# Kernel tuning notes

Hardware: AMD Instinct MI355X
Metric: run time of the kernel (lower is better)

The kernel has to match this reference:

```python
import jax, jax.numpy as jnp
import numpy as np

B, NP1, D = 64, 1025, 256  # N+1 tokens, feature dim d (label dim makes d+1)
N_LAYER, N_HEAD = 4, 4
VAR = 0.02


def _pad_pq(allparam):
    """Build padded (d+1)x(d+1) P_full/Q_full for all layers/heads at once.
    P_full gets a 1 at [d, d]; Q_full is zero-padded."""
    L, H, _, d, _ = allparam.shape
    Pf = (jnp.zeros((L, H, d + 1, d + 1), allparam.dtype)
          .at[:, :, :d, :d].set(allparam[:, :, 0])
          .at[:, :, d, d].set(1.0))
    Qf = (jnp.zeros((L, H, d + 1, d + 1), allparam.dtype)
          .at[:, :, :d, :d].set(allparam[:, :, 1]))
    return Pf, Qf


def setup_inputs() -> dict:
    key = jax.random.key(0)
    k1, k2 = jax.random.split(key)
    Z = jax.random.normal(k1, (B, NP1, D + 1), dtype=jnp.float32)
    allparam = jax.random.normal(k2, (N_LAYER, N_HEAD, 2, D, D), dtype=jnp.float32) * VAR
    return {"Z": Z, "allparam": allparam}


def reference(Z, allparam):
    Bb, Np1, dp1 = Z.shape
    N = Np1 - 1
    Pf, Qf = _pad_pq(allparam)  # (L, H, d+1, d+1)
    # mask A = diag(1,...,1,0): equivalent to zeroing the last key token
    mask = jnp.ones((Np1,), Z.dtype).at[N].set(0.0)
    for l in range(allparam.shape[0]):
        # attn[b,h,n,m] = Z[b,n,:] @ Q_full[h] @ Z[b,m,:]
        attn = jnp.einsum('bni,hij,bmj->bhnm', Z, Qf[l], Z)
        attn = jax.nn.relu(attn)
        # key[b,h,m,i] = P_full[h] @ Z[b,m,:], last token masked out (A matrix)
        key_t = jnp.einsum('hij,bmj->bhmi', Pf[l], Z) * mask[None, None, :, None]
        # sum over heads fused into the einsum reduction; scale by 1/N
        res = jnp.einsum('bhnm,bhmi->bni', attn, key_t) / N
        Z = Z + res  # residual connection
    return Z
```

## Files before the change

### kernel.cpp

```cpp
#include <hip/hip_runtime.h>
#include <cstdint>
#include <cstddef>

#define B_    64
#define NP1   1025
#define N_    1024
#define D_    256
#define DP1   257
#define L_    4
#define H_    4
#define MT    1024
#define NCHE  32
#define IPAD  272
#define TR_   1024

typedef __bf16 bf16;
typedef bf16 bf16x4 __attribute__((ext_vector_type(4)));
typedef bf16 bf16x8 __attribute__((ext_vector_type(8)));
typedef float f32x4 __attribute__((ext_vector_type(4)));

__device__ __forceinline__ f32x4 mfma16(bf16x8 a, bf16x8 b, f32x4 c) {
    return __builtin_amdgcn_mfma_f32_16x16x32_bf16(a, b, c, 0, 0, 0);
}

__device__ __forceinline__ void async16(const void* g, void* l) {
    __builtin_amdgcn_global_load_lds(
        (const __attribute__((address_space(1))) void*)g,
        (__attribute__((address_space(3))) void*)l, 16, 0, 0);
}

__global__ void k_prep_pq(const float* __restrict__ ap,
                          bf16* __restrict__ Pb, bf16* __restrict__ Qt) {
    int idx = blockIdx.x * 256 + threadIdx.x;
    int j  = idx & 255;
    int i  = (idx >> 8) & 255;
    int lh = idx >> 16;
    const float* base = ap + (size_t)lh * 2 * D_ * D_;
    float p = base[i * D_ + j];
    float q = base[D_ * D_ + i * D_ + j];
    Pb[((size_t)lh * D_ + i) * D_ + j] = (bf16)p;
    Qt[((size_t)lh * D_ + j) * D_ + i] = (bf16)q;
}

__global__ __launch_bounds__(256) void k_zbt(const float* __restrict__ Z,
                                             bf16* __restrict__ Zb,
                                             bf16* __restrict__ ZbT) {
    __shared__ float t[64][65];
    int m0 = blockIdx.x * 64, j0 = blockIdx.y * 64, b = blockIdx.z;
    int c = threadIdx.x & 63, r0 = threadIdx.x >> 6;
#pragma unroll
    for (int s = 0; s < 16; s++) {
        int r = s * 4 + r0;
        int j = j0 + c;
        float v = (j < DP1) ? Z[((size_t)b * NP1 + m0 + r) * DP1 + j] : 0.f;
        t[r][c] = v;
        if (j < D_) Zb[((size_t)b * N_ + m0 + r) * D_ + j] = (bf16)v;
    }
    __syncthreads();
#pragma unroll
    for (int s = 0; s < 16; s++) {
        int rr = s * 4 + r0;
        int j = j0 + rr;
        if (j < DP1)
            ZbT[((size_t)b * DP1 + j) * MT + m0 + c] = (bf16)t[c][rr];
    }
}

__global__ __launch_bounds__(512, 1) void k_attn(const bf16* __restrict__ Zb,
                                                 const bf16* __restrict__ ZbT,
                                                 const bf16* __restrict__ Qt,
                                                 const bf16* __restrict__ Pb,
                                                 float* __restrict__ Z,
                                                 bf16* __restrict__ T,
                                                 bf16* __restrict__ Tlab,
                                                 int layer) {
    __shared__ bf16 zbS[2][32][256];
    __shared__ bf16 ztS[2][IPAD][32];
    __shared__ bf16 sl[8][32][40];

    const int tid  = threadIdx.x;
    const int id   = blockIdx.x;
    const int wave = tid >> 6, lane = tid & 63;
    const int quad = lane >> 4, l16 = lane & 15;

    const int xcd = id & 7, u = id >> 3;
    const int b   = xcd + 8 * (u & 7);
    const int bx  = u >> 3;
    const int n0w = bx * 256 + wave * 32;

    const bf16* Zbb  = Zb  + (size_t)b * N_ * D_;
    const bf16* ZbTb = ZbT + (size_t)b * DP1 * MT;

    const int zrow  = wave * 2 + (lane >> 5);
    const int zscol = ((lane & 31) ^ (zrow & 7)) * 8;
    const int krow  = wave * 16 + (lane >> 2);
    const int kscol = ((lane & 3) ^ ((lane >> 3) & 3)) * 8;
    const int xs    = l16 & 7;
    const int kf    = (l16 >> 1) & 3;

    auto stage = [&](int mc_, int p_) {
        int m0 = mc_ * 32;
        const bf16* zsrc = Zbb + (size_t)(m0 + zrow) * D_ + zscol;
#pragma unroll
        for (int t = 0; t < 2; t++)
            async16(zsrc + (size_t)t * 16 * D_, &zbS[p_][t * 16 + wave * 2][0]);
        const bf16* ksrc = ZbTb + (size_t)krow * MT + m0 + kscol;
#pragma unroll
        for (int t = 0; t < 2; t++)
            async16(ksrc + (size_t)t * 128 * MT, &ztS[p_][t * 128 + wave * 16][0]);
        if (wave == 0)
            async16(ksrc + (size_t)256 * MT, &ztS[p_][256][0]);
    };

    int p = 0;

    for (int h = 0; h < H_; h++) {
        const bf16* Qth = Qt + (size_t)(layer * H_ + h) * D_ * D_;

        if (h == 0) stage(0, 0);

        f32x4 acc[2][17];
#pragma unroll
        for (int ns = 0; ns < 2; ns++)
#pragma unroll
            for (int it = 0; it < 17; it++) acc[ns][it] = (f32x4){0.f, 0.f, 0.f, 0.f};

        bf16x8 zqa[2][8];
#pragma unroll 2
        for (int jc = 0; jc < 8; jc++) {
            f32x4 c00 = (f32x4){0.f,0.f,0.f,0.f}, c01 = c00, c10 = c00, c11 = c00;
#pragma unroll
            for (int kc = 0; kc < 8; kc++) {
                const bf16* qb = Qth + (size_t)(jc * 32 + l16) * D_ + kc * 32 + quad * 8;
                const bf16* az = Zbb + (size_t)(n0w + l16) * D_ + kc * 32 + quad * 8;
                bf16x8 q0 = *(const bf16x8*)(qb);
                bf16x8 q1 = *(const bf16x8*)(qb + 16 * D_);
                bf16x8 a0 = *(const bf16x8*)(az);
                bf16x8 a1 = *(const bf16x8*)(az + 16 * D_);
                c00 = mfma16(q0, a0, c00);
                c01 = mfma16(q0, a1, c01);
                c10 = mfma16(q1, a0, c10);
                c11 = mfma16(q1, a1, c11);
            }
            f32x4 cv[2][2] = {{c00, c01}, {c10, c11}};
#pragma unroll
            for (int jt = 0; jt < 2; jt++)
#pragma unroll
                for (int ns = 0; ns < 2; ns++) {
                    bf16x4 pk;
#pragma unroll
                    for (int r = 0; r < 4; r++) pk[r] = (bf16)cv[jt][ns][r];
                    *(bf16x4*)(&sl[wave][ns * 16 + l16][jt * 16 + quad * 4]) = pk;
                }
#pragma unroll
            for (int ns = 0; ns < 2; ns++)
                zqa[ns][jc] = *(const bf16x8*)(&sl[wave][ns * 16 + l16][quad * 8]);
        }

        if (h == 0) {
            asm volatile("s_waitcnt vmcnt(0)" ::: "memory");
            __builtin_amdgcn_s_barrier();
            __builtin_amdgcn_sched_barrier(0);
        }

        for (int cc = 0; cc < NCHE; cc++) {
            const bool haveNext = (cc + 1 < NCHE);
            if (haveNext) {
                int mcn = (h & 1) ? (NCHE - 2 - cc) : (cc + 1);
                stage(mcn, p ^ 1);
                if (wave == 0) asm volatile("s_waitcnt vmcnt(5)" ::: "memory");
                else           asm volatile("s_waitcnt vmcnt(4)" ::: "memory");
            } else {
                asm volatile("s_waitcnt vmcnt(0)" ::: "memory");
            }
            __builtin_amdgcn_s_barrier();
            __builtin_amdgcn_sched_barrier(0);

#pragma unroll
            for (int mt = 0; mt < 2; mt++) {
                f32x4 st0 = (f32x4){0.f,0.f,0.f,0.f}, st1 = st0;
                const bf16* zr = &zbS[p][mt * 16 + l16][0];
                __builtin_amdgcn_s_setprio(1);
#pragma unroll
                for (int kc = 0; kc < 8; kc++) {
                    bf16x8 az = *(const bf16x8*)(zr + (((kc * 4 + quad) ^ xs) * 8));
                    st0 = mfma16(az, zqa[0][kc], st0);
                    st1 = mfma16(az, zqa[1][kc], st1);
                }
                __builtin_amdgcn_s_setprio(0);
                bf16x4 p0, p1;
#pragma unroll
                for (int r = 0; r < 4; r++) {
                    p0[r] = (bf16)(st0[r] > 0.f ? st0[r] : 0.f);
                    p1[r] = (bf16)(st1[r] > 0.f ? st1[r] : 0.f);
                }
                *(bf16x4*)(&sl[wave][l16][mt * 16 + quad * 4])      = p0;
                *(bf16x4*)(&sl[wave][16 + l16][mt * 16 + quad * 4]) = p1;
            }
            bf16x8 sfrag[2];
#pragma unroll
            for (int ns = 0; ns < 2; ns++)
                sfrag[ns] = *(const bf16x8*)(&sl[wave][ns * 16 + l16][quad * 8]);

            __builtin_amdgcn_s_setprio(1);
#pragma unroll
            for (int it = 0; it < 17; it++) {
                const bf16* kr = &ztS[p][it * 16 + l16][0];
                bf16x8 bk = *(const bf16x8*)(kr + ((quad ^ kf) * 8));
                acc[0][it] = mfma16(sfrag[0], bk, acc[0][it]);
                acc[1][it] = mfma16(sfrag[1], bk, acc[1][it]);
            }
            __builtin_amdgcn_s_setprio(0);

            __builtin_amdgcn_sched_barrier(0);
            __builtin_amdgcn_s_barrier();
            if (haveNext) p ^= 1;
        }

        bf16* Th  = T    + (size_t)(b * H_ + h) * TR_ * D_;
        bf16* Tlh = Tlab + (size_t)(b * H_ + h) * TR_;
#pragma unroll
        for (int ns = 0; ns < 2; ns++)
#pragma unroll
            for (int it = 0; it < 17; it++)
#pragma unroll
                for (int r = 0; r < 4; r++) {
                    int n = n0w + ns * 16 + quad * 4 + r;
                    float v = acc[ns][it][r];
                    if (it < 16)
                        Th[(size_t)n * D_ + it * 16 + l16] = (bf16)v;
                    else if (l16 == 0)
                        Tlh[n] = (bf16)v;
                }
    }

    if (bx == 0) {
        __syncthreads();
        float* lz1 = (float*)&zbS[0][0][0];
        float* lzq = lz1 + 256;
        float* lsS = lzq + 1024;
        float* lT  = lsS + 4096;
        if (tid < 256) lz1[tid] = Z[((size_t)b * NP1 + N_) * DP1 + tid];
        __syncthreads();
        {
            int j = tid & 255, hh = tid >> 8;
            for (int h2 = hh; h2 < H_; h2 += 2) {
                const bf16* qr = Qt + ((size_t)(layer * H_ + h2) * D_ + j) * D_;
                float a = 0.f;
                for (int i8 = 0; i8 < 32; i8++) {
                    bf16x8 q = *(const bf16x8*)(qr + i8 * 8);
#pragma unroll
                    for (int k = 0; k < 8; k++) a += lz1[i8 * 8 + k] * (float)q[k];
                }
                lzq[h2 * 256 + j] = a;
            }
        }
        __syncthreads();
        for (int m = tid; m < N_; m += 512) {
            const bf16* zr = Zbb + (size_t)m * D_;
            float a0 = 0.f, a1 = 0.f, a2 = 0.f, a3 = 0.f;
            for (int j8 = 0; j8 < 32; j8++) {
                bf16x8 z8 = *(const bf16x8*)(zr + j8 * 8);
#pragma unroll
                for (int k = 0; k < 8; k++) {
                    float zv = (float)z8[k];
                    int j = j8 * 8 + k;
                    a0 += lzq[j] * zv;
                    a1 += lzq[256 + j] * zv;
                    a2 += lzq[512 + j] * zv;
                    a3 += lzq[768 + j] * zv;
                }
            }
            lsS[m]        = a0 > 0.f ? a0 : 0.f;
            lsS[1024 + m] = a1 > 0.f ? a1 : 0.f;
            lsS[2048 + m] = a2 > 0.f ? a2 : 0.f;
            lsS[3072 + m] = a3 > 0.f ? a3 : 0.f;
        }
        __syncthreads();
        if (tid < DP1) {
            const bf16* tr2 = ZbTb + (size_t)tid * MT;
            float t0 = 0.f, t1 = 0.f, t2 = 0.f, t3 = 0.f;
            for (int m8 = 0; m8 < 128; m8++) {
                bf16x8 t8 = *(const bf16x8*)(tr2 + m8 * 8);
#pragma unroll
                for (int k = 0; k < 8; k++) {
                    float zv = (float)t8[k];
                    int m = m8 * 8 + k;
                    t0 += lsS[m] * zv;
                    t1 += lsS[1024 + m] * zv;
                    t2 += lsS[2048 + m] * zv;
                    t3 += lsS[3072 + m] * zv;
                }
            }
            lT[tid] = t0; lT[257 + tid] = t1; lT[514 + tid] = t2; lT[771 + tid] = t3;
        }
        __syncthreads();
        const float inv = 1.0f / (float)N_;
        if (tid < 256) {
            float out = 0.f;
            for (int h2 = 0; h2 < H_; h2++) {
                const bf16* pr = Pb + ((size_t)(layer * H_ + h2) * D_ + tid) * D_;
                for (int j8 = 0; j8 < 32; j8++) {
                    bf16x8 p8 = *(const bf16x8*)(pr + j8 * 8);
#pragma unroll
                    for (int k = 0; k < 8; k++)
                        out += lT[h2 * 257 + j8 * 8 + k] * (float)p8[k];
                }
            }
            Z[((size_t)b * NP1 + N_) * DP1 + tid] += out * inv;
        } else if (tid == 256) {
            float lab = lT[256] + lT[513] + lT[770] + lT[1027];
            Z[((size_t)b * NP1 + N_) * DP1 + D_] += lab * inv;
        }
    }
}

__global__ __launch_bounds__(256, 4) void k_post(const bf16* __restrict__ T,
                                                 const bf16* __restrict__ Tlab,
                                                 const bf16* __restrict__ Pb,
                                                 float* __restrict__ Z,
                                                 bf16* __restrict__ Zb,
                                                 bf16* __restrict__ ZbT,
                                                 int layer) {
    const int tid  = threadIdx.x;
    const int id   = blockIdx.x;
    const int wave = tid >> 6, lane = tid & 63;
    const int quad = lane >> 4, l16 = lane & 15;
    const int xcd = id & 7, u = id >> 3;
    const int b   = xcd + 8 * (u & 3) + 32 * ((u >> 5) & 1);
    const int bx  = (u >> 2) & 7;
    const int ih  = u >> 6;
    const int n0w = bx * 128 + wave * 32;
    const int i0  = ih * 128;

    f32x4 acc[2][8];
#pragma unroll
    for (int ns = 0; ns < 2; ns++)
#pragma unroll
        for (int it = 0; it < 8; it++) acc[ns][it] = (f32x4){0.f, 0.f, 0.f, 0.f};

    for (int h = 0; h < H_; h++) {
        const bf16* Th = T  + (size_t)(b * H_ + h) * TR_ * D_;
        const bf16* Ph = Pb + (size_t)(layer * H_ + h) * D_ * D_;
#pragma unroll 2
        for (int kc = 0; kc < 8; kc++) {
            bf16x8 af[2];
#pragma unroll
            for (int ns = 0; ns < 2; ns++) {
                int row = n0w + ns * 16 + l16;
                af[ns] = *(const bf16x8*)(Th + (size_t)row * D_ + kc * 32 + quad * 8);
            }
#pragma unroll
            for (int it = 0; it < 8; it++) {
                bf16x8 bp = *(const bf16x8*)(Ph + (size_t)(i0 + it * 16 + l16) * D_ + kc * 32 + quad * 8);
                acc[0][it] = mfma16(af[0], bp, acc[0][it]);
                acc[1][it] = mfma16(af[1], bp, acc[1][it]);
            }
        }
    }

    const float inv = 1.0f / (float)N_;
    const bool wnext = (layer < L_ - 1);
#pragma unroll
    for (int ns = 0; ns < 2; ns++)
#pragma unroll
        for (int it = 0; it < 8; it++) {
            const int i = i0 + it * 16 + l16;
            const int nbase = n0w + ns * 16 + quad * 4;
            bf16x4 zpk;
#pragma unroll
            for (int r = 0; r < 4; r++) {
                int n = nbase + r;
                size_t zi = ((size_t)b * NP1 + n) * DP1 + i;
                float v = Z[zi] + acc[ns][it][r] * inv;
                Z[zi] = v;
                zpk[r] = (bf16)v;
                if (wnext) Zb[((size_t)b * N_ + n) * D_ + i] = (bf16)v;
            }
            if (wnext)
                *(bf16x4*)(&ZbT[((size_t)b * DP1 + i) * MT + nbase]) = zpk;
        }
    if (ih == 0 && tid < 128) {
        int n = bx * 128 + tid;
        float s = 0.f;
#pragma unroll
        for (int h = 0; h < H_; h++)
            s += (float)Tlab[(size_t)(b * H_ + h) * TR_ + n];
        size_t zi = ((size_t)b * NP1 + n) * DP1 + D_;
        float v = Z[zi] + s * inv;
        Z[zi] = v;
        if (wnext) ZbT[((size_t)b * DP1 + D_) * MT + n] = (bf16)v;
    }
}

extern "C" void kernel_launch(void* const* d_in, const int* in_sizes, int n_in,
                              void* d_out, int out_size, void* d_ws, size_t ws_size,
                              hipStream_t stream) {
    const float* Zin = (const float*)d_in[0];
    const float* ap  = (const float*)d_in[1];
    float* Z = (float*)d_out;

    char* ws = (char*)d_ws;
    const size_t sz_Zb  = (size_t)B_ * N_ * D_ * sizeof(bf16);
    const size_t sz_ZbT = (size_t)B_ * DP1 * MT * sizeof(bf16);
    const size_t sz_T   = (size_t)B_ * H_ * TR_ * D_ * sizeof(bf16);
    const size_t sz_Tl  = (size_t)B_ * H_ * TR_ * sizeof(bf16);
    const size_t sz_P   = (size_t)L_ * H_ * D_ * D_ * sizeof(bf16);
    bf16* Zb  = (bf16*)ws;
    bf16* ZbT = (bf16*)(ws + sz_Zb);
    bf16* Tb  = (bf16*)(ws + sz_Zb + sz_ZbT);
    bf16* Tl  = (bf16*)(ws + sz_Zb + sz_ZbT + sz_T);
    bf16* Pb  = (bf16*)(ws + sz_Zb + sz_ZbT + sz_T + sz_Tl);
    bf16* Qt  = (bf16*)(ws + sz_Zb + sz_ZbT + sz_T + sz_Tl + sz_P);

    hipMemcpyAsync(Z, Zin, (size_t)B_ * NP1 * DP1 * sizeof(float),
                   hipMemcpyDeviceToDevice, stream);

    k_prep_pq<<<dim3((L_ * H_ * D_ * D_) / 256), 256, 0, stream>>>(ap, Pb, Qt);
    k_zbt<<<dim3(N_ / 64, 5, B_), 256, 0, stream>>>(Z, Zb, ZbT);

    for (int l = 0; l < L_; l++) {
        k_attn<<<dim3(256), 512, 0, stream>>>(Zb, ZbT, Qt, Pb, Z, Tb, Tl, l);
        k_post<<<dim3(1024), 256, 0, stream>>>(Tb, Tl, Pb, Z, Zb, ZbT, l);
    }
}
```

Measured before the change: 3.326 ms.

## Fuse P-projection residual update into attention kernel and regenerate bf16 copies with k_zbt

This removes the separate k_post kernel. Each attention block now runs the P-projection over its own 256 token rows right after writing T, and adds the result into Z in place, including the label column. The bf16 copies Zb and ZbT for the next layer are no longer written by the epilogue. Instead the existing k_zbt transpose kernel is launched between layers. The aim is to save a launch and the global round trip of the separate post pass. In exchange, the projection now runs on only 256 blocks instead of 1024, and a 128-float accumulator per thread may raise register pressure.

```diff
diff --git a/kernel.cpp b/kernel.cpp
--- a/kernel.cpp
+++ b/kernel.cpp
@@ -232,6 +232,57 @@
                     else if (l16 == 0)
                         Tlh[n] = (bf16)v;
                 }
+    }
+
+    __syncthreads();
+    {
+        f32x4 acc2[2][16];
+#pragma unroll
+        for (int ns = 0; ns < 2; ns++)
+#pragma unroll
+            for (int it = 0; it < 16; it++) acc2[ns][it] = (f32x4){0.f, 0.f, 0.f, 0.f};
+
+        for (int h = 0; h < H_; h++) {
+            const bf16* Th = T  + (size_t)(b * H_ + h) * TR_ * D_;
+            const bf16* Ph = Pb + (size_t)(layer * H_ + h) * D_ * D_;
+#pragma unroll 2
+            for (int kc = 0; kc < 8; kc++) {
+                bf16x8 af[2];
+#pragma unroll
+                for (int ns = 0; ns < 2; ns++) {
+                    int row = n0w + ns * 16 + l16;
+                    af[ns] = *(const bf16x8*)(Th + (size_t)row * D_ + kc * 32 + quad * 8);
+                }
+#pragma unroll
+                for (int it = 0; it < 16; it++) {
+                    bf16x8 bp = *(const bf16x8*)(Ph + (size_t)(it * 16 + l16) * D_ + kc * 32 + quad * 8);
+                    acc2[0][it] = mfma16(af[0], bp, acc2[0][it]);
+                    acc2[1][it] = mfma16(af[1], bp, acc2[1][it]);
+                }
+            }
+        }
+
+        const float inv = 1.0f / (float)N_;
+#pragma unroll
+        for (int ns = 0; ns < 2; ns++)
+#pragma unroll
+            for (int it = 0; it < 16; it++) {
+                const int i = it * 16 + l16;
+                const int nbase = n0w + ns * 16 + quad * 4;
+#pragma unroll
+                for (int r = 0; r < 4; r++) {
+                    size_t zi = ((size_t)b * NP1 + nbase + r) * DP1 + i;
+                    Z[zi] += acc2[ns][it][r] * inv;
+                }
+            }
+        if (tid < 256) {
+            int n = bx * 256 + tid;
+            float s = 0.f;
+#pragma unroll
+            for (int h = 0; h < H_; h++)
+                s += (float)Tlab[(size_t)(b * H_ + h) * TR_ + n];
+            Z[((size_t)b * NP1 + n) * DP1 + D_] += s * inv;
+        }
     }
 
     if (bx == 0) {
@@ -315,84 +366,6 @@
     }
 }
 
-__global__ __launch_bounds__(256, 4) void k_post(const bf16* __restrict__ T,
-                                                 const bf16* __restrict__ Tlab,
-                                                 const bf16* __restrict__ Pb,
-                                                 float* __restrict__ Z,
-                                                 bf16* __restrict__ Zb,
-                                                 bf16* __restrict__ ZbT,
-                                                 int layer) {
-    const int tid  = threadIdx.x;
-    const int id   = blockIdx.x;
-    const int wave = tid >> 6, lane = tid & 63;
-    const int quad = lane >> 4, l16 = lane & 15;
-    const int xcd = id & 7, u = id >> 3;
-    const int b   = xcd + 8 * (u & 3) + 32 * ((u >> 5) & 1);
-    const int bx  = (u >> 2) & 7;
-    const int ih  = u >> 6;
-    const int n0w = bx * 128 + wave * 32;
-    const int i0  = ih * 128;
-
-    f32x4 acc[2][8];
-#pragma unroll
-    for (int ns = 0; ns < 2; ns++)
-#pragma unroll
-        for (int it = 0; it < 8; it++) acc[ns][it] = (f32x4){0.f, 0.f, 0.f, 0.f};
-
-    for (int h = 0; h < H_; h++) {
-        const bf16* Th = T  + (size_t)(b * H_ + h) * TR_ * D_;
-        const bf16* Ph = Pb + (size_t)(layer * H_ + h) * D_ * D_;
-#pragma unroll 2
-        for (int kc = 0; kc < 8; kc++) {
-            bf16x8 af[2];
-#pragma unroll
-            for (int ns = 0; ns < 2; ns++) {
-                int row = n0w + ns * 16 + l16;
-                af[ns] = *(const bf16x8*)(Th + (size_t)row * D_ + kc * 32 + quad * 8);
-            }
-#pragma unroll
-            for (int it = 0; it < 8; it++) {
-                bf16x8 bp = *(const bf16x8*)(Ph + (size_t)(i0 + it * 16 + l16) * D_ + kc * 32 + quad * 8);
-                acc[0][it] = mfma16(af[0], bp, acc[0][it]);
-                acc[1][it] = mfma16(af[1], bp, acc[1][it]);
-            }
-        }
-    }
-
-    const float inv = 1.0f / (float)N_;
-    const bool wnext = (layer < L_ - 1);
-#pragma unroll
-    for (int ns = 0; ns < 2; ns++)
-#pragma unroll
-        for (int it = 0; it < 8; it++) {
-            const int i = i0 + it * 16 + l16;
-            const int nbase = n0w + ns * 16 + quad * 4;
-            bf16x4 zpk;
-#pragma unroll
-            for (int r = 0; r < 4; r++) {
-                int n = nbase + r;
-                size_t zi = ((size_t)b * NP1 + n) * DP1 + i;
-                float v = Z[zi] + acc[ns][it][r] * inv;
-                Z[zi] = v;
-                zpk[r] = (bf16)v;
-                if (wnext) Zb[((size_t)b * N_ + n) * D_ + i] = (bf16)v;
-            }
-            if (wnext)
-                *(bf16x4*)(&ZbT[((size_t)b * DP1 + i) * MT + nbase]) = zpk;
-        }
-    if (ih == 0 && tid < 128) {
-        int n = bx * 128 + tid;
-        float s = 0.f;
-#pragma unroll
-        for (int h = 0; h < H_; h++)
-            s += (float)Tlab[(size_t)(b * H_ + h) * TR_ + n];
-        size_t zi = ((size_t)b * NP1 + n) * DP1 + D_;
-        float v = Z[zi] + s * inv;
-        Z[zi] = v;
-        if (wnext) ZbT[((size_t)b * DP1 + D_) * MT + n] = (bf16)v;
-    }
-}
-
 extern "C" void kernel_launch(void* const* d_in, const int* in_sizes, int n_in,
                               void* d_out, int out_size, void* d_ws, size_t ws_size,
                               hipStream_t stream) {
@@ -421,6 +394,7 @@
 
     for (int l = 0; l < L_; l++) {
         k_attn<<<dim3(256), 512, 0, stream>>>(Zb, ZbT, Qt, Pb, Z, Tb, Tl, l);
-        k_post<<<dim3(1024), 256, 0, stream>>>(Tb, Tl, Pb, Z, Zb, ZbT, l);
-    }
-}
+        if (l < L_ - 1)
+            k_zbt<<<dim3(N_ / 64, 5, B_), 256, 0, stream>>>(Z, Zb, ZbT);
+    }
+}
```

Measured after the change: 3.199 ms. 1.04x faster.
